# Performance work log

Hardware: AMD Instinct MI355X
Metric: run time of the kernel (lower is better)

## Reference

```python
import jax, jax.numpy as jnp
import numpy as np

NEG_INF = -1e9


def setup_inputs() -> dict:
    key = jax.random.key(0)
    k1, k2, k3 = jax.random.split(key, 3)
    B, C, Q, D = 32, 2048, 128, 128
    context = jax.random.normal(k1, (B, C, D), dtype=jnp.float32)
    query = jax.random.normal(k2, (B, Q, D), dtype=jnp.float32)
    # Dense(1, use_bias=False) over concat([c, q, c*q]) -> weight vector of length 3*D
    w = jax.random.normal(k3, (3 * D,), dtype=jnp.float32) * (1.0 / np.sqrt(3 * D))
    query_mask = jnp.ones((B, Q), dtype=jnp.int32)
    return {"context": context, "query": query, "w": w, "query_mask": query_mask}


def reference(context, query, w, query_mask):
    # context: [B, C, D], query: [B, Q, D], w: [3D], query_mask: [B, Q]
    D = context.shape[-1]
    w1, w2, w3 = w[:D], w[D:2 * D], w[2 * D:]
    # Trilinear similarity, exactly equal to Dense(1)(concat([c_tiled, q_tiled, c*q]))
    # S[b,c,q] = context[b,c]·w1 + query[b,q]·w2 + (context[b,c]*w3)·query[b,q]
    S = (context @ w1)[:, :, None] \
        + (query @ w2)[:, None, :] \
        + jnp.einsum('bcd,bqd->bcq', context * w3, query)  # [B, C, Q]
    mask_add = (1.0 - query_mask.astype(jnp.float32))[:, None, :] * NEG_INF
    S = S + mask_add
    a = jax.nn.softmax(S, axis=2)                  # context-to-query attention [B, C, Q]
    c2q = jnp.einsum('bcq,bqd->bcd', a, query)     # [B, C, D]
    b = jax.nn.softmax(jnp.max(S, axis=2), axis=1) # query-to-context weights [B, C]
    q2c = jnp.einsum('bc,bcd->bd', b, context)[:, None, :]  # [B, 1, D]
    q2c = jnp.broadcast_to(q2c, context.shape)     # tile over c_len
    out = jnp.concatenate([context, c2q, context * c2q, context * q2c], axis=-1)
    return out  # [B, C, 4D]
```

## Files before the change

kernel.cpp:

```cpp
#include <hip/hip_runtime.h>
#include <cstdint>

#define B_ 32
#define C_ 2048
#define Q_ 128
#define D_ 128
#define CT 64
#define OFF_ 8.0f
#define NEG_INF_F (-1.0e9f)

typedef __attribute__((ext_vector_type(8))) short bf16x8;
typedef __attribute__((ext_vector_type(4))) float f32x4;

__device__ inline short bf16_rne(float v) {
    unsigned u = __float_as_uint(v);
    return (short)((u + 0x7FFFu + ((u >> 16) & 1u)) >> 16);
}
__device__ inline void split_f32(float v, short& h, short& l) {
    unsigned u  = __float_as_uint(v);
    unsigned hb = u & 0xffff0000u;
    float lo = v - __uint_as_float(hb);
    h = (short)(hb >> 16);
    l = (short)(__float_as_uint(lo) >> 16);
}

__global__ __launch_bounds__(256)
void cqa_prep(const float* __restrict__ qry, const float* __restrict__ w,
              const int* __restrict__ qmask, float* __restrict__ qw2e_g,
              unsigned short* __restrict__ qw3Hi, unsigned short* __restrict__ qTHi)
{
    const int b = blockIdx.y, ch = blockIdx.x;
    const int t = threadIdx.x;
    const float* qb = qry + (size_t)b * Q_ * D_;

    if (t < 32) {
        int rl = t >> 1, part = t & 1;
        int q = ch * 16 + rl;
        const float* p  = qb + q * D_ + part * 64;
        const float* wp = w + D_ + part * 64;
        float s = 0.f;
        #pragma unroll
        for (int j = 0; j < 64; j += 4) {
            float4 a4 = *(const float4*)(p + j);
            float4 w4 = *(const float4*)(wp + j);
            s += a4.x*w4.x + a4.y*w4.y + a4.z*w4.z + a4.w*w4.w;
        }
        s += __shfl_xor(s, 1, 2);
        if (!part) {
            float madd = (1.0f - (float)qmask[b * Q_ + q]) * NEG_INF_F;
            qw2e_g[b * Q_ + q] = s + madd;
        }
    }
    #pragma unroll
    for (int i = 0; i < 8; ++i) {
        int idx = t + i * 256;
        int ql = idx >> 7, d = idx & 127;
        int q = ch * 16 + ql;
        float v = qb[q * D_ + d];
        qw3Hi[((size_t)b * Q_ + q) * D_ + d] = (unsigned short)bf16_rne(v * w[2 * D_ + d]);
        qTHi[((size_t)b * D_ + d) * Q_ + q]  = (unsigned short)bf16_rne(v);
    }
}

__device__ __forceinline__ void stage_b(const unsigned short* __restrict__ gH,
                                        int col0, short* sb, int wv, int lane)
{
    #pragma unroll
    for (int j = 0; j < 2; ++j) {
        int seg = wv * 2 + j;
        int li  = seg * 64 + lane;
        int row = li >> 2;
        int col = (li & 3) * 8;
        __builtin_amdgcn_global_load_lds(
            (const __attribute__((address_space(1))) void*)(gH + (size_t)row * 128 + col0 + col),
            (__attribute__((address_space(3))) void*)(sb + seg * 512), 16, 0, 0);
    }
}

__global__ __launch_bounds__(256, 4)
void cqa_main(const float* __restrict__ ctx, const float* __restrict__ w,
              const float* __restrict__ qw2e_g,
              const unsigned short* __restrict__ qw3Hi, const unsigned short* __restrict__ qTHi,
              float* __restrict__ out, float* __restrict__ part, float* __restrict__ denp_g)
{
    __shared__ __align__(16) char smem[34176];
    short* SB   = (short*)smem;
    short* PHi  = (short*)smem;
    float* Tr   = (float*)smem;
    float* red  = (float*)smem;
    float* mlds = (float*)(smem + 32768);
    float* slds = (float*)(smem + 33024);
    float* cw1  = (float*)(smem + 33280);
    float* qw2e = (float*)(smem + 33536);
    float* dred = (float*)(smem + 34048);

    const int b   = blockIdx.y;
    const int c0  = blockIdx.x * CT;
    const int tid = threadIdx.x;
    const int lane = tid & 63;
    const int wv   = tid >> 6;
    const int w16  = wv * 16;
    const int lm   = lane & 15;
    const int lg   = lane >> 4;
    const int lk   = lg * 8;

    const float* ctxb = ctx + ((size_t)b * C_ + c0) * D_;
    const unsigned short* qw3Hb = qw3Hi + (size_t)b * Q_ * D_;
    const unsigned short* qTHb  = qTHi + (size_t)b * Q_ * D_;

    #pragma unroll
    for (int t = 0; t < 4; ++t)
        stage_b(qw3Hb, t * 32, SB + t * 4096, wv, lane);

    if (tid < Q_) qw2e[tid] = qw2e_g[b * Q_ + tid];

    const float* arow = ctxb + (size_t)(w16 + lm) * D_;
    bf16x8 aHr[4], aLr[4];
    float cws = 0.f;
    #pragma unroll
    for (int t = 0; t < 4; ++t) {
        float4 v0 = *(const float4*)(arow + t * 32 + lk);
        float4 v1 = *(const float4*)(arow + t * 32 + lk + 4);
        float4 w0 = *(const float4*)(w + t * 32 + lk);
        float4 w1v = *(const float4*)(w + t * 32 + lk + 4);
        cws += v0.x*w0.x + v0.y*w0.y + v0.z*w0.z + v0.w*w0.w
             + v1.x*w1v.x + v1.y*w1v.y + v1.z*w1v.z + v1.w*w1v.w;
        float vv[8] = {v0.x, v0.y, v0.z, v0.w, v1.x, v1.y, v1.z, v1.w};
        #pragma unroll
        for (int i = 0; i < 8; ++i) {
            short hh, ll; split_f32(vv[i], hh, ll);
            aHr[t][i] = hh; aLr[t][i] = ll;
        }
    }
    cws += __shfl_xor(cws, 16, 64);
    cws += __shfl_xor(cws, 32, 64);
    if (lane < 16) cw1[w16 + lm] = cws;
    __syncthreads();

    float qe[8];
    #pragma unroll
    for (int f = 0; f < 8; ++f) qe[f] = qw2e[f * 16 + lm];
    float cwr[4];
    #pragma unroll
    for (int r = 0; r < 4; ++r) cwr[r] = cw1[w16 + lg * 4 + r];

    const f32x4 vzero = {0.f, 0.f, 0.f, 0.f};
    f32x4 acc[8];
    #pragma unroll
    for (int f = 0; f < 8; ++f) acc[f] = vzero;

    #pragma unroll
    for (int t = 0; t < 4; ++t) {
        const short* sb = SB + t * 4096;
        bf16x8 aH = aHr[t], aL = aLr[t];
        #pragma unroll
        for (int f = 0; f < 8; ++f) {
            bf16x8 bH = *(const bf16x8*)(sb + (f * 16 + lm) * 32 + lk);
            acc[f] = __builtin_amdgcn_mfma_f32_16x16x32_bf16(aH, bH, acc[f], 0, 0, 0);
            acc[f] = __builtin_amdgcn_mfma_f32_16x16x32_bf16(aL, bH, acc[f], 0, 0, 0);
        }
    }
    __syncthreads();

    bf16x8 qa[2][4];
    #pragma unroll
    for (int ds = 0; ds < 2; ++ds)
        #pragma unroll
        for (int t = 0; t < 4; ++t)
            qa[ds][t] = *(const bf16x8*)(qTHb + (size_t)(ds * 64 + w16 + lm) * 128 + t * 32 + lk);

    #pragma unroll
    for (int r = 0; r < 4; ++r) {
        float sv[8];
        float mx = -3.0e38f;
        #pragma unroll
        for (int f = 0; f < 8; ++f) {
            sv[f] = acc[f][r] + qe[f];
            mx = fmaxf(mx, sv[f]);
        }
        mx = fmaxf(mx, __shfl_xor(mx, 1, 16));
        mx = fmaxf(mx, __shfl_xor(mx, 2, 16));
        mx = fmaxf(mx, __shfl_xor(mx, 4, 16));
        mx = fmaxf(mx, __shfl_xor(mx, 8, 16));
        int lrow = w16 + lg * 4 + r;
        float s = 0.f;
        #pragma unroll
        for (int f = 0; f < 8; ++f) {
            float p = __expf(sv[f] - mx);
            s += p;
            PHi[lrow * 136 + f * 16 + lm] = bf16_rne(p);
        }
        s += __shfl_xor(s, 1, 16);
        s += __shfl_xor(s, 2, 16);
        s += __shfl_xor(s, 4, 16);
        s += __shfl_xor(s, 8, 16);
        if (lm == 0) { mlds[lrow] = mx + cwr[r]; slds[lrow] = 1.0f / s; }
    }
    __syncthreads();

    f32x4 acc2[2][4];
    #pragma unroll
    for (int ds = 0; ds < 2; ++ds)
        #pragma unroll
        for (int fc = 0; fc < 4; ++fc) acc2[ds][fc] = vzero;

    #pragma unroll
    for (int t = 0; t < 4; ++t) {
        #pragma unroll
        for (int fc = 0; fc < 4; ++fc) {
            bf16x8 bP = *(const bf16x8*)(PHi + (fc * 16 + lm) * 136 + t * 32 + lk);
            acc2[0][fc] = __builtin_amdgcn_mfma_f32_16x16x32_bf16(qa[0][t], bP, acc2[0][fc], 0, 0, 0);
            acc2[1][fc] = __builtin_amdgcn_mfma_f32_16x16x32_bf16(qa[1][t], bP, acc2[1][fc], 0, 0, 0);
        }
    }
    __syncthreads();

    const int rsel = tid >> 5;
    const int dd   = (tid & 31) * 4;
    float4 qacc = {0.f, 0.f, 0.f, 0.f};
    float denp = 0.f;
    #pragma unroll
    for (int p = 0; p < 2; ++p) {
        #pragma unroll
        for (int fq = 0; fq < 2; ++fq) {
            int fc = 2 * p + fq;
            float ic = slds[fc * 16 + lm];
            int cl = fq * 16 + lm;
            #pragma unroll
            for (int ds = 0; ds < 2; ++ds) {
                f32x4 v = acc2[ds][fc];
                float4 o;
                o.x = v[0] * ic; o.y = v[1] * ic; o.z = v[2] * ic; o.w = v[3] * ic;
                *(float4*)(Tr + cl * 132 + ds * 64 + w16 + lg * 4) = o;
            }
        }
        __syncthreads();
        #pragma unroll
        for (int i = 0; i < 4; ++i) {
            int cl  = i * 8 + rsel;
            int row = p * 32 + cl;
            float4 a  = *(const float4*)(Tr + cl * 132 + dd);
            float4 cv = *(const float4*)(ctxb + (size_t)row * D_ + dd);
            float wgt = __expf(mlds[row] - OFF_);
            size_t obase = ((size_t)b * C_ + c0 + row) * (4 * D_);
            float4 pr;
            pr.x = cv.x*a.x; pr.y = cv.y*a.y; pr.z = cv.z*a.z; pr.w = cv.w*a.w;
            *(float4*)(out + obase + dd)          = cv;
            *(float4*)(out + obase + D_ + dd)     = a;
            *(float4*)(out + obase + 2 * D_ + dd) = pr;
            qacc.x += wgt * cv.x; qacc.y += wgt * cv.y;
            qacc.z += wgt * cv.z; qacc.w += wgt * cv.w;
            denp += wgt;
        }
        __syncthreads();
    }

    *(float4*)(red + rsel * 128 + dd) = qacc;
    if ((tid & 31) == 0) dred[rsel] = denp;
    __syncthreads();
    if (tid < 128) {
        float s = 0.f;
        #pragma unroll
        for (int rr = 0; rr < 8; ++rr) s += red[rr * 128 + tid];
        part[((size_t)b * 32 + blockIdx.x) * 128 + tid] = s;
    }
    if (tid == 0) {
        float s = 0.f;
        #pragma unroll
        for (int rr = 0; rr < 8; ++rr) s += dred[rr];
        denp_g[b * 32 + blockIdx.x] = s;
    }
}

__global__ __launch_bounds__(256)
void cqa_out4(const float* __restrict__ ctx, const float* __restrict__ part,
              const float* __restrict__ denp_g, float* __restrict__ out)
{
    const int b = blockIdx.y, ch = blockIdx.x;
    const int tid = threadIdx.x;
    __shared__ float q2s[128];

    float den = 0.f;
    #pragma unroll 8
    for (int j = 0; j < 32; ++j) den += denp_g[b * 32 + j];
    if (tid < 128) {
        float s = 0.f;
        #pragma unroll 8
        for (int j = 0; j < 32; ++j) s += part[((size_t)b * 32 + j) * 128 + tid];
        q2s[tid] = s / den;
    }
    __syncthreads();

    const float* cb = ctx + ((size_t)b * C_ + ch * 64) * D_;
    float* ob = out + ((size_t)b * C_ + ch * 64) * (4 * D_);
    #pragma unroll
    for (int k = 0; k < 8; ++k) {
        int i  = tid + k * 256;
        int rl = i >> 5, d4 = (i & 31) * 4;
        float4 c4 = *(const float4*)(cb + (size_t)rl * D_ + d4);
        float4 g4 = *(const float4*)(q2s + d4);
        float4 o;
        o.x = c4.x*g4.x; o.y = c4.y*g4.y; o.z = c4.z*g4.z; o.w = c4.w*g4.w;
        *(float4*)(ob + (size_t)rl * (4 * D_) + 3 * D_ + d4) = o;
    }
}

extern "C" void kernel_launch(void* const* d_in, const int* in_sizes, int n_in,
                              void* d_out, int out_size, void* d_ws, size_t ws_size,
                              hipStream_t stream)
{
    const float* ctx   = (const float*)d_in[0];
    const float* qry   = (const float*)d_in[1];
    const float* w     = (const float*)d_in[2];
    const int*   qmask = (const int*)d_in[3];
    float* out = (float*)d_out;
    float* ws  = (float*)d_ws;

    float* part    = ws;
    float* denp_g  = ws + 131072;
    float* qw2e_g  = ws + 132096;
    unsigned short* bf = (unsigned short*)(ws + 136192);
    unsigned short* qw3Hi = bf;
    unsigned short* qTHi  = bf + 524288;

    cqa_prep<<<dim3(8, B_), 256, 0, stream>>>(qry, w, qmask, qw2e_g, qw3Hi, qTHi);
    cqa_main<<<dim3(C_/CT, B_), 256, 0, stream>>>(ctx, w, qw2e_g, qw3Hi, qTHi,
                                                  out, part, denp_g);
    cqa_out4<<<dim3(C_/64, B_), 256, 0, stream>>>(ctx, part, denp_g, out);
}
```

Measured before the change: 52.75 us.

## Swizzle block-to-batch mapping, hoist query loads, split PV MFMA per output pass

Remaps the linear block id so that consecutive blocks are spread across batches, likely to balance work across XCDs and L2 caches. Issues the qT fragment global loads before the first barrier so their latency overlaps the score MFMAs. Also splits the P·V MFMA into two halves computed inside each output pass, with the transpose buffer moved to a separate LDS region so it does not overwrite P. This raises LDS use slightly and may reduce occupancy or raise register pressure.

```diff
diff --git a/kernel.cpp b/kernel.cpp
--- a/kernel.cpp
+++ b/kernel.cpp
@@ -22,6 +22,11 @@
     float lo = v - __uint_as_float(hb);
     h = (short)(hb >> 16);
     l = (short)(__float_as_uint(lo) >> 16);
+}
+
+__device__ __forceinline__ void swz(int id, int& b, int& cch) {
+    b   = (id & 7) * 4 + (id >> 8);
+    cch = (id >> 3) & 31;
 }
 
 __global__ __launch_bounds__(256)
@@ -83,19 +88,20 @@
               const unsigned short* __restrict__ qw3Hi, const unsigned short* __restrict__ qTHi,
               float* __restrict__ out, float* __restrict__ part, float* __restrict__ denp_g)
 {
-    __shared__ __align__(16) char smem[34176];
+    __shared__ __align__(16) char smem[35648];
     short* SB   = (short*)smem;
     short* PHi  = (short*)smem;
-    float* Tr   = (float*)smem;
+    float* Tr   = (float*)(smem + 17408);
     float* red  = (float*)smem;
-    float* mlds = (float*)(smem + 32768);
-    float* slds = (float*)(smem + 33024);
-    float* cw1  = (float*)(smem + 33280);
-    float* qw2e = (float*)(smem + 33536);
-    float* dred = (float*)(smem + 34048);
-
-    const int b   = blockIdx.y;
-    const int c0  = blockIdx.x * CT;
+    float* mlds = (float*)(smem + 34304);
+    float* slds = (float*)(smem + 34560);
+    float* cw1  = (float*)(smem + 34816);
+    float* qw2e = (float*)(smem + 35072);
+    float* dred = (float*)(smem + 35584);
+
+    int b, cch;
+    swz(blockIdx.y * 32 + blockIdx.x, b, cch);
+    const int c0  = cch * CT;
     const int tid = threadIdx.x;
     const int lane = tid & 63;
     const int wv   = tid >> 6;
@@ -135,6 +141,14 @@
     cws += __shfl_xor(cws, 16, 64);
     cws += __shfl_xor(cws, 32, 64);
     if (lane < 16) cw1[w16 + lm] = cws;
+
+    bf16x8 qa[2][4];
+    #pragma unroll
+    for (int ds = 0; ds < 2; ++ds)
+        #pragma unroll
+        for (int t = 0; t < 4; ++t)
+            qa[ds][t] = *(const bf16x8*)(qTHb + (size_t)(ds * 64 + w16 + lm) * 128 + t * 32 + lk);
+
     __syncthreads();
 
     float qe[8];
@@ -161,13 +175,6 @@
         }
     }
     __syncthreads();
-
-    bf16x8 qa[2][4];
-    #pragma unroll
-    for (int ds = 0; ds < 2; ++ds)
-        #pragma unroll
-        for (int t = 0; t < 4; ++t)
-            qa[ds][t] = *(const bf16x8*)(qTHb + (size_t)(ds * 64 + w16 + lm) * 128 + t * 32 + lk);
 
     #pragma unroll
     for (int r = 0; r < 4; ++r) {
@@ -198,37 +205,33 @@
     }
     __syncthreads();
 
-    f32x4 acc2[2][4];
-    #pragma unroll
-    for (int ds = 0; ds < 2; ++ds)
-        #pragma unroll
-        for (int fc = 0; fc < 4; ++fc) acc2[ds][fc] = vzero;
-
-    #pragma unroll
-    for (int t = 0; t < 4; ++t) {
-        #pragma unroll
-        for (int fc = 0; fc < 4; ++fc) {
-            bf16x8 bP = *(const bf16x8*)(PHi + (fc * 16 + lm) * 136 + t * 32 + lk);
-            acc2[0][fc] = __builtin_amdgcn_mfma_f32_16x16x32_bf16(qa[0][t], bP, acc2[0][fc], 0, 0, 0);
-            acc2[1][fc] = __builtin_amdgcn_mfma_f32_16x16x32_bf16(qa[1][t], bP, acc2[1][fc], 0, 0, 0);
-        }
-    }
-    __syncthreads();
-
     const int rsel = tid >> 5;
     const int dd   = (tid & 31) * 4;
     float4 qacc = {0.f, 0.f, 0.f, 0.f};
     float denp = 0.f;
     #pragma unroll
     for (int p = 0; p < 2; ++p) {
+        f32x4 acc2[2][2];
+        #pragma unroll
+        for (int ds = 0; ds < 2; ++ds)
+            #pragma unroll
+            for (int fq = 0; fq < 2; ++fq) acc2[ds][fq] = vzero;
+        #pragma unroll
+        for (int t = 0; t < 4; ++t) {
+            #pragma unroll
+            for (int fq = 0; fq < 2; ++fq) {
+                bf16x8 bP = *(const bf16x8*)(PHi + ((2*p+fq) * 16 + lm) * 136 + t * 32 + lk);
+                acc2[0][fq] = __builtin_amdgcn_mfma_f32_16x16x32_bf16(qa[0][t], bP, acc2[0][fq], 0, 0, 0);
+                acc2[1][fq] = __builtin_amdgcn_mfma_f32_16x16x32_bf16(qa[1][t], bP, acc2[1][fq], 0, 0, 0);
+            }
+        }
         #pragma unroll
         for (int fq = 0; fq < 2; ++fq) {
-            int fc = 2 * p + fq;
-            float ic = slds[fc * 16 + lm];
+            float ic = slds[(2*p+fq) * 16 + lm];
             int cl = fq * 16 + lm;
             #pragma unroll
             for (int ds = 0; ds < 2; ++ds) {
-                f32x4 v = acc2[ds][fc];
+                f32x4 v = acc2[ds][fq];
                 float4 o;
                 o.x = v[0] * ic; o.y = v[1] * ic; o.z = v[2] * ic; o.w = v[3] * ic;
                 *(float4*)(Tr + cl * 132 + ds * 64 + w16 + lg * 4) = o;
@@ -262,13 +265,13 @@
         float s = 0.f;
         #pragma unroll
         for (int rr = 0; rr < 8; ++rr) s += red[rr * 128 + tid];
-        part[((size_t)b * 32 + blockIdx.x) * 128 + tid] = s;
+        part[((size_t)b * 32 + cch) * 128 + tid] = s;
     }
     if (tid == 0) {
         float s = 0.f;
         #pragma unroll
         for (int rr = 0; rr < 8; ++rr) s += dred[rr];
-        denp_g[b * 32 + blockIdx.x] = s;
+        denp_g[b * 32 + cch] = s;
     }
 }
 
@@ -276,7 +279,8 @@
 void cqa_out4(const float* __restrict__ ctx, const float* __restrict__ part,
               const float* __restrict__ denp_g, float* __restrict__ out)
 {
-    const int b = blockIdx.y, ch = blockIdx.x;
+    int b, ch;
+    swz(blockIdx.y * 32 + blockIdx.x, b, ch);
     const int tid = threadIdx.x;
     __shared__ float q2s[128];
 
```

Result: no change. 51.83 us (median of 2 runs) (-1.7%).
